# Kernel tuning notes

Hardware: AMD Instinct MI355X
Metric: run time of the kernel (lower is better)

The kernel has to match this reference:

```python
import jax, jax.numpy as jnp
import numpy as np

B, N, K = 4, 4096, 16
DP, DM = 64, 128
EPS = 1e-8


def setup_inputs() -> dict:
    key = jax.random.key(0)
    ks = jax.random.split(key, 32)
    g = lambda i, shape, fan: jax.random.normal(ks[i], shape, jnp.float32) / np.sqrt(fan)
    inp = {
        'xyz': jax.random.normal(ks[0], (B, N, 3), jnp.float32),
        'features': jax.random.normal(ks[1], (B, N, DP), jnp.float32),
        # fc1: d_points -> d_model
        'fc1_w': g(2, (DP, DM), DP), 'fc1_b': jnp.zeros((DM,), jnp.float32),
        # fc2: d_model -> d_points
        'fc2_w': g(3, (DM, DP), DM), 'fc2_b': jnp.zeros((DP,), jnp.float32),
        # fc_delta: Linear(3,DM) -> ReLU -> Linear(DM,DM)
        'd1_w': g(4, (3, DM), 3), 'd1_b': jnp.zeros((DM,), jnp.float32),
        'd2_w': g(5, (DM, DM), DM), 'd2_b': jnp.zeros((DM,), jnp.float32),
        # fc_gamma: Linear(DM,DM) -> ReLU -> Linear(DM,DM)
        'g1_w': g(6, (DM, DM), DM), 'g1_b': jnp.zeros((DM,), jnp.float32),
        'g2_w': g(7, (DM, DM), DM), 'g2_b': jnp.zeros((DM,), jnp.float32),
        # q/k/v projections, no bias
        'wq_w': g(8, (DM, DM), DM), 'wk_w': g(9, (DM, DM), DM), 'wv_w': g(10, (DM, DM), DM),
        # fc_sim: Linear(DM+1, DM)
        'sim_w': g(11, (DM + 1, DM), DM + 1), 'sim_b': jnp.zeros((DM,), jnp.float32),
    }
    return inp


def _gather(t, idx):
    # t: [B, N, C], idx: [B, N, K] -> [B, N, K, C]
    bidx = jnp.arange(t.shape[0])[:, None, None]
    return t[bidx, idx]


def reference(xyz, features, fc1_w, fc1_b, fc2_w, fc2_b, d1_w, d1_b, d2_w, d2_b,
              g1_w, g1_b, g2_w, g2_b, wq_w, wk_w, wv_w, sim_w, sim_b):
    # pairwise squared distances [B, N, N]
    sq = jnp.sum(xyz * xyz, axis=-1)
    dists = sq[:, :, None] + sq[:, None, :] - 2.0 * jnp.einsum('bnc,bmc->bnm', xyz, xyz)
    knn_idx = jnp.argsort(dists, axis=-1)[:, :, :K]            # [B, N, K]

    knn_xyz = _gather(xyz, knn_idx)                            # [B, N, K, 3]
    x = features @ fc1_w + fc1_b                               # [B, N, DM]
    q = x @ wq_w                                               # [B, N, DM]
    k = _gather(x @ wk_w, knn_idx)                             # [B, N, K, DM]
    v = _gather(x @ wv_w, knn_idx)                             # [B, N, K, DM]

    rel_pos = xyz[:, :, None, :] - knn_xyz                     # [B, N, K, 3]
    pos_enc = jax.nn.relu(rel_pos @ d1_w + d1_b) @ d2_w + d2_b # [B, N, K, DM]

    qe = q[:, :, None, :]                                      # [B, N, 1, DM]
    # torch cosine_similarity: dot / (max(||q||,eps) * max(||k||,eps))
    qn = jnp.maximum(jnp.linalg.norm(q, axis=-1), EPS)[:, :, None]
    kn = jnp.maximum(jnp.linalg.norm(k, axis=-1), EPS)
    sim = jnp.sum(qe * k, axis=-1) / (qn * kn)                 # [B, N, K]

    rel_qk = jnp.concatenate([sim[..., None], qe - k], axis=-1)  # [B, N, K, DM+1]
    rel_qk = rel_qk @ sim_w + sim_b                            # [B, N, K, DM]

    attn = jax.nn.relu((rel_qk + pos_enc) @ g1_w + g1_b) @ g2_w + g2_b
    attn = jax.nn.softmax(attn / np.sqrt(DM).astype(np.float32), axis=-2)  # over K

    res = jnp.einsum('bnkf,bnkf->bnf', attn, v + pos_enc)      # [B, N, DM]
    res = res @ fc2_w + fc2_b + features                       # [B, N, DP]
    return res, attn
```

## Files before the change

### kernel.cpp

```cpp
#include <hip/hip_runtime.h>
#include <hip/hip_bf16.h>

#define BB 4
#define NN 4096
#define KK 16
#define DP 64
#define DM 128
#define DMP 132
#define SPITCH 264
#define EPSF 1e-8f
#define OUT0N ((size_t)BB * NN * DP)

typedef unsigned short u16t;
typedef __attribute__((ext_vector_type(8))) short s8v;
typedef __attribute__((ext_vector_type(4))) float f4v;

__device__ int g_flag;

__device__ __forceinline__ float u2f(u16t u) {
    unsigned int x = ((unsigned int)u) << 16;
    return __uint_as_float(x);
}
__device__ __forceinline__ u16t f2u(float v) {
    __hip_bfloat16 h = __float2bfloat16(v);
    return *(u16t*)&h;
}
__device__ __forceinline__ void splitf(float x, u16t& h, u16t& l) {
    const unsigned xb = __float_as_uint(x);
    h = (u16t)(xb >> 16);
    const float hf = __uint_as_float(xb & 0xffff0000u);
    l = (u16t)(__float_as_uint(x - hf) >> 16);
}

template<int DT> struct IO;
template<> struct IO<0> {
    static __device__ __forceinline__ float ld(const void* p, size_t i) { return ((const float*)p)[i]; }
    static __device__ __forceinline__ void ld4(const void* p, size_t i, float o[4]) {
        float4 v = *(const float4*)((const float*)p + i);
        o[0] = v.x; o[1] = v.y; o[2] = v.z; o[3] = v.w;
    }
    static __device__ __forceinline__ void st(void* p, size_t i, float v) { ((float*)p)[i] = v; }
};
template<> struct IO<1> {
    static __device__ __forceinline__ float ld(const void* p, size_t i) { return u2f(((const u16t*)p)[i]); }
    static __device__ __forceinline__ void ld4(const void* p, size_t i, float o[4]) {
        ushort4 v = *(const ushort4*)((const u16t*)p + i);
        o[0] = u2f(v.x); o[1] = u2f(v.y); o[2] = u2f(v.z); o[3] = u2f(v.w);
    }
    static __device__ __forceinline__ void st(void* p, size_t i, float v) { ((u16t*)p)[i] = f2u(v); }
};

__global__ __launch_bounds__(64) void detect_kernel(const void* feat) {
    const int tid = threadIdx.x;
    float x = u2f(((const u16t*)feat)[2 * tid]);
    float a = fabsf(x);
    bool sane = (x == 0.0f) || (a > 1e-4f && a < 50.0f);
    unsigned long long m = __ballot(sane);
    if (tid == 0) g_flag = (__popcll(m) >= 32) ? 1 : 0;
}

struct QkvSmem { float sf[DP]; float sx[DM]; };

template<int DT>
__device__ __forceinline__ void qkv_body(QkvSmem& s,
    const void* feat, const void* fc1_w, const void* fc1_b,
    const void* wq, const void* wk, const void* wv,
    float* __restrict__ qbuf, float* __restrict__ kbuf, float* __restrict__ vbuf)
{
    const int bn = blockIdx.x;
    const int tid = threadIdx.x;
    if (tid < DP) s.sf[tid] = IO<DT>::ld(feat, (size_t)bn * DP + tid);
    __syncthreads();
    float x = IO<DT>::ld(fc1_b, tid);
#pragma unroll 4
    for (int i = 0; i < DP; i++) x = fmaf(s.sf[i], IO<DT>::ld(fc1_w, i * DM + tid), x);
    s.sx[tid] = x;
    __syncthreads();
    float q = 0.f, k = 0.f, v = 0.f;
    for (int i0 = 0; i0 < DM; i0 += 4) {
        float4 xv = *(const float4*)&s.sx[i0];
        const float xs[4] = { xv.x, xv.y, xv.z, xv.w };
#pragma unroll
        for (int j = 0; j < 4; j++) {
            q = fmaf(xs[j], IO<DT>::ld(wq, (i0 + j) * DM + tid), q);
            k = fmaf(xs[j], IO<DT>::ld(wk, (i0 + j) * DM + tid), k);
            v = fmaf(xs[j], IO<DT>::ld(wv, (i0 + j) * DM + tid), v);
        }
    }
    qbuf[(size_t)bn * DM + tid] = q;
    kbuf[(size_t)bn * DM + tid] = k;
    vbuf[(size_t)bn * DM + tid] = v;
}

__global__ __launch_bounds__(128) void qkv_kernel(
    const void* feat, const void* fc1_w, const void* fc1_b,
    const void* wq, const void* wk, const void* wv,
    float* qbuf, float* kbuf, float* vbuf)
{
    __shared__ __align__(16) QkvSmem s;
    if (g_flag) qkv_body<1>(s, feat, fc1_w, fc1_b, wq, wk, wv, qbuf, kbuf, vbuf);
    else        qkv_body<0>(s, feat, fc1_w, fc1_b, wq, wk, wv, qbuf, kbuf, vbuf);
}

struct Qkv16Smem { float sf[16][DP]; float sx[16][DMP]; };

template<int DT>
__device__ __forceinline__ void qkv16_body(Qkv16Smem& s,
    const void* feat, const void* fc1_w, const void* fc1_b,
    const void* wq, const void* wk, const void* wv,
    float* __restrict__ qbuf, float* __restrict__ kbuf, float* __restrict__ vbuf)
{
    const int pnt0 = blockIdx.x << 4;
    const int tid = threadIdx.x;
    {
        const int r = tid >> 4, c4 = (tid & 15) << 2;
        float o[4];
        IO<DT>::ld4(feat, (size_t)(pnt0 + r) * DP + c4, o);
        s.sf[r][c4 + 0] = o[0]; s.sf[r][c4 + 1] = o[1];
        s.sf[r][c4 + 2] = o[2]; s.sf[r][c4 + 3] = o[3];
    }
    __syncthreads();
    const int c = tid & 127, h = tid >> 7;
    {
        float acc[8];
        const float fb = IO<DT>::ld(fc1_b, c);
#pragma unroll
        for (int pp = 0; pp < 8; pp++) acc[pp] = fb;
        for (int i = 0; i < DP; i++) {
            const float w = IO<DT>::ld(fc1_w, (size_t)i * DM + c);
#pragma unroll
            for (int pp = 0; pp < 8; pp++) acc[pp] = fmaf(s.sf[h * 8 + pp][i], w, acc[pp]);
        }
#pragma unroll
        for (int pp = 0; pp < 8; pp++) s.sx[h * 8 + pp][c] = acc[pp];
    }
    __syncthreads();
    {
        float aq[8], ak[8], av[8];
#pragma unroll
        for (int pp = 0; pp < 8; pp++) { aq[pp] = 0.f; ak[pp] = 0.f; av[pp] = 0.f; }
        for (int i0 = 0; i0 < DM; i0 += 4) {
            float x4[8][4];
#pragma unroll
            for (int pp = 0; pp < 8; pp++) {
                const float4 xv = *(const float4*)&s.sx[h * 8 + pp][i0];
                x4[pp][0] = xv.x; x4[pp][1] = xv.y; x4[pp][2] = xv.z; x4[pp][3] = xv.w;
            }
#pragma unroll
            for (int j = 0; j < 4; j++) {
                const float wqv = IO<DT>::ld(wq, (size_t)(i0 + j) * DM + c);
                const float wkv = IO<DT>::ld(wk, (size_t)(i0 + j) * DM + c);
                const float wvv = IO<DT>::ld(wv, (size_t)(i0 + j) * DM + c);
#pragma unroll
                for (int pp = 0; pp < 8; pp++) {
                    aq[pp] = fmaf(x4[pp][j], wqv, aq[pp]);
                    ak[pp] = fmaf(x4[pp][j], wkv, ak[pp]);
                    av[pp] = fmaf(x4[pp][j], wvv, av[pp]);
                }
            }
        }
#pragma unroll
        for (int pp = 0; pp < 8; pp++) {
            const size_t row = (size_t)(pnt0 + h * 8 + pp) * DM + c;
            qbuf[row] = aq[pp]; kbuf[row] = ak[pp]; vbuf[row] = av[pp];
        }
    }
}

__global__ __launch_bounds__(256) void qkv16_kernel(
    const void* feat, const void* fc1_w, const void* fc1_b,
    const void* wq, const void* wk, const void* wv,
    float* qbuf, float* kbuf, float* vbuf)
{
    __shared__ __align__(16) Qkv16Smem s;
    if (g_flag) qkv16_body<1>(s, feat, fc1_w, fc1_b, wq, wk, wv, qbuf, kbuf, vbuf);
    else        qkv16_body<0>(s, feat, fc1_w, fc1_b, wq, wk, wv, qbuf, kbuf, vbuf);
}

template<int DT>
__device__ __forceinline__ void knn_body(float4* __restrict__ sc,
    const void* xyz, int* dst, int dstride, void* dout, int in_out)
{
    if (in_out) {
        if (DT) { dst = (int*)((u16t*)dout + OUT0N); dstride = (KK * DM) / 2; }
        else    { dst = (int*)((float*)dout + OUT0N); dstride = KK * DM; }
    }
    const int b = blockIdx.x >> 8;
    const int tid = threadIdx.x;
    for (int j = tid; j < NN; j += 512) {
        float x = IO<DT>::ld(xyz, ((size_t)b * NN + j) * 3 + 0);
        float y = IO<DT>::ld(xyz, ((size_t)b * NN + j) * 3 + 1);
        float z = IO<DT>::ld(xyz, ((size_t)b * NN + j) * 3 + 2);
        float sq = __fadd_rn(__fadd_rn(__fmul_rn(x, x), __fmul_rn(y, y)), __fmul_rn(z, z));
        sc[j] = make_float4(x, y, z, sq);
    }
    __syncthreads();
    const int lane = tid & 63;
    const int wave = tid >> 6;

    for (int qi = 0; qi < 2; qi++) {
        const int r = ((blockIdx.x & 255) << 4) + (wave << 1) + qi;
        const float4 qc = sc[r];

        float d[KK];
        int id[KK];
#pragma unroll
        for (int t = 0; t < KK; t++) { d[t] = 3.4e38f; id[t] = 0x7fffffff; }

        for (int j = lane; j < NN; j += 64) {
            const float4 c = sc[j];
            const float dot = __fadd_rn(__fadd_rn(__fmul_rn(qc.x, c.x), __fmul_rn(qc.y, c.y)),
                                        __fmul_rn(qc.z, c.z));
            const float dist = __fsub_rn(__fadd_rn(qc.w, c.w), __fmul_rn(2.0f, dot));
            if (dist < d[KK - 1]) {
                float cd = dist; int ci = j;
#pragma unroll
                for (int t = 0; t < KK; t++) {
                    const bool sw = (cd < d[t]);
                    const float od = d[t]; const int oi = id[t];
                    d[t]  = sw ? cd : d[t];
                    id[t] = sw ? ci : id[t];
                    cd = sw ? od : cd;
                    ci = sw ? oi : ci;
                }
            }
        }

        const size_t base = (size_t)(b * NN + r) * (size_t)dstride;
#pragma unroll
        for (int t = 0; t < KK; t++) {
            float bd = d[0]; int bi = id[0];
#pragma unroll
            for (int off = 32; off >= 1; off >>= 1) {
                const float od = __shfl_xor(bd, off, 64);
                const int   oi = __shfl_xor(bi, off, 64);
                if (od < bd || (od == bd && oi < bi)) { bd = od; bi = oi; }
            }
            const bool win = (d[0] == bd) && (id[0] == bi);
            if (win) {
#pragma unroll
                for (int u = 0; u < KK - 1; u++) { d[u] = d[u + 1]; id[u] = id[u + 1]; }
                d[KK - 1] = 3.4e38f; id[KK - 1] = 0x7fffffff;
            }
            if (lane == t) dst[base + t] = bi;
        }
    }
}

__global__ __launch_bounds__(512) void knn_kernel(
    const void* xyz, int* dst, int dstride, void* dout, int in_out)
{
    __shared__ __align__(16) float4 sc[NN];
    if (g_flag) knn_body<1>(sc, xyz, dst, dstride, dout, in_out);
    else        knn_body<0>(sc, xyz, dst, dstride, dout, in_out);
}

template<int DT>
__device__ __forceinline__ void gemm_tile(const float* __restrict__ IN,
                                          const void* __restrict__ W, int woff,
                                          int kg, int f0, float acc[4][4])
{
#pragma unroll
    for (int a = 0; a < 4; a++)
#pragma unroll
        for (int c = 0; c < 4; c++) acc[a][c] = 0.f;
    for (int i0 = 0; i0 < DM; i0 += 4) {
        float w[4][4];
#pragma unroll
        for (int j = 0; j < 4; j++) IO<DT>::ld4(W, (size_t)woff + (i0 + j) * DM + f0, w[j]);
#pragma unroll
        for (int kk = 0; kk < 4; kk++) {
            float4 x4 = *(const float4*)(IN + (kg * 4 + kk) * DMP + i0);
            const float xs[4] = { x4.x, x4.y, x4.z, x4.w };
#pragma unroll
            for (int ff = 0; ff < 4; ff++)
#pragma unroll
                for (int j = 0; j < 4; j++)
                    acc[kk][ff] = fmaf(xs[j], w[j][ff], acc[kk][ff]);
        }
    }
}

template<int DT>
__device__ __forceinline__ void wprep_body(const void* sim_w, const void* d2_w,
                                           const void* g1_w, const void* g2_w,
                                           u16t* __restrict__ wprep)
{
    const int m  = blockIdx.x >> 3;
    const int t  = blockIdx.x & 7;
    const int ks = threadIdx.x >> 6;
    const int lane = threadIdx.x & 63;
    const void* src = (m == 0) ? sim_w : (m == 1) ? d2_w : (m == 2) ? g1_w : g2_w;
    const int srcoff = (m == 0) ? DM : 0;
    u16t* hi = wprep + (size_t)m * 32768;
    u16t* lo = hi + 16384;
    const int c  = t * 16 + (lane & 15);
    const int k0 = ks * 32 + ((lane >> 4) << 3);
    s8v vh, vl;
#pragma unroll
    for (int j = 0; j < 8; j++) {
        const float x = IO<DT>::ld(src, (size_t)srcoff + (size_t)(k0 + j) * DM + c);
        const u16t h = f2u(x);
        vh[j] = (short)h;
        vl[j] = (short)f2u(x - u2f(h));
    }
    const size_t off = ((size_t)(t * 4 + ks) * 64 + lane) * 8;
    *(s8v*)(hi + off) = vh;
    *(s8v*)(lo + off) = vl;
}

__global__ __launch_bounds__(256) void wprep_kernel(
    const void* sim_w, const void* d2_w, const void* g1_w, const void* g2_w,
    u16t* wprep)
{
    if (g_flag) wprep_body<1>(sim_w, d2_w, g1_w, g2_w, wprep);
    else        wprep_body<0>(sim_w, d2_w, g1_w, g2_w, wprep);
}

__device__ __forceinline__ void mfma_g(const u16t* __restrict__ SP,
                                       const u16t* __restrict__ wmat,
                                       int lane, int w, f4v acc[4][2])
{
    const u16t* whi = wmat;
    const u16t* wlo = wmat + 16384;
    const int arow = lane & 15;
    const int ak   = (lane >> 4) << 3;
#pragma unroll
    for (int ks = 0; ks < 4; ks++) {
        const size_t o0 = ((size_t)(((2 * w + 0) * 4 + ks) * 64) + lane) * 8;
        const size_t o1 = ((size_t)(((2 * w + 1) * 4 + ks) * 64) + lane) * 8;
        const s8v b0h = *(const s8v*)(whi + o0);
        const s8v b0l = *(const s8v*)(wlo + o0);
        const s8v b1h = *(const s8v*)(whi + o1);
        const s8v b1l = *(const s8v*)(wlo + o1);
#pragma unroll
        for (int m = 0; m < 4; m++) {
            const u16t* ar = SP + (size_t)(m * 16 + arow) * SPITCH + ak + ks * 32;
            const s8v ah = *(const s8v*)ar;
            const s8v al = *(const s8v*)(ar + 128);
            acc[m][0] = __builtin_amdgcn_mfma_f32_16x16x32_bf16(ah, b0h, acc[m][0], 0, 0, 0);
            acc[m][0] = __builtin_amdgcn_mfma_f32_16x16x32_bf16(ah, b0l, acc[m][0], 0, 0, 0);
            acc[m][0] = __builtin_amdgcn_mfma_f32_16x16x32_bf16(al, b0h, acc[m][0], 0, 0, 0);
            acc[m][1] = __builtin_amdgcn_mfma_f32_16x16x32_bf16(ah, b1h, acc[m][1], 0, 0, 0);
            acc[m][1] = __builtin_amdgcn_mfma_f32_16x16x32_bf16(ah, b1l, acc[m][1], 0, 0, 0);
            acc[m][1] = __builtin_amdgcn_mfma_f32_16x16x32_bf16(al, b1h, acc[m][1], 0, 0, 0);
        }
    }
}

struct Attn5Smem {
    u16t  SP[64 * SPITCH];
    float sq[4][DM];
    float sres[4][DM];
    float ssim[64];
};

template<int DT>
__device__ __forceinline__ void attn5_body(Attn5Smem& s,
    const void* xyz, const void* feat,
    const void* fc2_w, const void* fc2_b,
    const void* d1_w, const void* d1_b, const void* d2_b,
    const void* g1_b, const void* g2_b,
    const void* sim_w, const void* sim_b,
    const float* __restrict__ qbuf, const float* __restrict__ kbuf,
    const float* __restrict__ vbuf,
    const int* __restrict__ knn, const u16t* __restrict__ wprep, void* dout)
{
    void* out0 = dout;
    void* out1 = DT ? (void*)((u16t*)dout + OUT0N) : (void*)((float*)dout + OUT0N);
    const int pnt0 = blockIdx.x << 2;
    const int b = pnt0 >> 12;
    const int tid = threadIdx.x;
    const int lane = tid & 63;
    const int w = tid >> 6;
    const int h = lane >> 4;
    const int c = lane & 15;
    const int row = tid >> 2;
    const int cb  = (tid & 3) << 5;

    int sv = knn[(size_t)(pnt0 + w) * KK + (row & 15)];
    sv = (sv < 0) ? 0 : (sv > NN - 1 ? NN - 1 : sv);
    const int grow = (b << 12) + sv;
    const float rx = IO<DT>::ld(xyz, (size_t)(pnt0 + w) * 3 + 0) - IO<DT>::ld(xyz, (size_t)grow * 3 + 0);
    const float ry = IO<DT>::ld(xyz, (size_t)(pnt0 + w) * 3 + 1) - IO<DT>::ld(xyz, (size_t)grow * 3 + 1);
    const float rz = IO<DT>::ld(xyz, (size_t)(pnt0 + w) * 3 + 2) - IO<DT>::ld(xyz, (size_t)grow * 3 + 2);
    float4 kreg[8];
#pragma unroll
    for (int j4 = 0; j4 < 8; j4++)
        kreg[j4] = *(const float4*)&kbuf[(size_t)grow * DM + cb + 4 * j4];
    const float2 q2 = *(const float2*)&qbuf[(size_t)(pnt0 + w) * DM + lane * 2];
    *(float2*)&s.sq[w][lane * 2] = q2;
    float qq = fmaf(q2.x, q2.x, q2.y * q2.y);
#pragma unroll
    for (int off = 1; off <= 32; off <<= 1) qq += __shfl_xor(qq, off, 64);
    const float qn = fmaxf(sqrtf(qq), EPSF);

    {
        u16t* hp = &s.SP[row * SPITCH];
#pragma unroll
        for (int j4 = 0; j4 < 32; j4 += 4) {
            float w0[4], w1[4], w2[4], bb[4];
            IO<DT>::ld4(d1_w, (size_t)0 * DM + cb + j4, w0);
            IO<DT>::ld4(d1_w, (size_t)1 * DM + cb + j4, w1);
            IO<DT>::ld4(d1_w, (size_t)2 * DM + cb + j4, w2);
            IO<DT>::ld4(d1_b, cb + j4, bb);
            ushort4 hv, lv;
#pragma unroll
            for (int jj = 0; jj < 4; jj++) {
                const float hx = fmaxf(fmaf(rz, w2[jj], fmaf(ry, w1[jj], fmaf(rx, w0[jj], bb[jj]))), 0.f);
                u16t hs, ls; splitf(hx, hs, ls);
                ((u16t*)&hv)[jj] = hs; ((u16t*)&lv)[jj] = ls;
            }
            *(ushort4*)(hp + cb + j4) = hv;
            *(ushort4*)(hp + 128 + cb + j4) = lv;
        }
    }
    __syncthreads();

    f4v pe[4][2] = { { {0,0,0,0},{0,0,0,0} }, { {0,0,0,0},{0,0,0,0} },
                     { {0,0,0,0},{0,0,0,0} }, { {0,0,0,0},{0,0,0,0} } };
    mfma_g(s.SP, wprep + 1 * 32768, lane, w, pe);
#pragma unroll
    for (int nt = 0; nt < 2; nt++) {
        const float bv = IO<DT>::ld(d2_b, (2 * w + nt) * 16 + c);
#pragma unroll
        for (int m = 0; m < 4; m++)
#pragma unroll
            for (int r = 0; r < 4; r++) pe[m][nt][r] += bv;
    }
    {
        float sk = 0.f, sd = 0.f;
#pragma unroll
        for (int j4 = 0; j4 < 8; j4++) {
            const float4 kv = kreg[j4];
            const float4 qv = *(const float4*)&s.sq[w][cb + 4 * j4];
            sk = fmaf(kv.x, kv.x, fmaf(kv.y, kv.y, fmaf(kv.z, kv.z, fmaf(kv.w, kv.w, sk))));
            sd = fmaf(qv.x, kv.x, fmaf(qv.y, kv.y, fmaf(qv.z, kv.z, fmaf(qv.w, kv.w, sd))));
        }
        sk += __shfl_xor(sk, 1, 64); sk += __shfl_xor(sk, 2, 64);
        sd += __shfl_xor(sd, 1, 64); sd += __shfl_xor(sd, 2, 64);
        if ((tid & 3) == 0) {
            const float kn = fmaxf(sqrtf(sk), EPSF);
            s.ssim[row] = sd / (qn * kn);
        }
    }
    __syncthreads();

    {
        u16t* hp = &s.SP[row * SPITCH];
#pragma unroll
        for (int j4 = 0; j4 < 8; j4++) {
            const float4 kv = kreg[j4];
            const float4 qv = *(const float4*)&s.sq[w][cb + 4 * j4];
            ushort4 hv, lv;
            splitf(qv.x - kv.x, hv.x, lv.x);
            splitf(qv.y - kv.y, hv.y, lv.y);
            splitf(qv.z - kv.z, hv.z, lv.z);
            splitf(qv.w - kv.w, hv.w, lv.w);
            *(ushort4*)(hp + cb + 4 * j4) = hv;
            *(ushort4*)(hp + 128 + cb + 4 * j4) = lv;
        }
    }
    __syncthreads();

    {
        f4v a1[4][2] = { { {0,0,0,0},{0,0,0,0} }, { {0,0,0,0},{0,0,0,0} },
                         { {0,0,0,0},{0,0,0,0} }, { {0,0,0,0},{0,0,0,0} } };
        mfma_g(s.SP, wprep + 0 * 32768, lane, w, a1);
        __syncthreads();
#pragma unroll
        for (int nt = 0; nt < 2; nt++) {
            const int col = (2 * w + nt) * 16 + c;
            const float bv  = IO<DT>::ld(sim_b, col);
            const float w0v = IO<DT>::ld(sim_w, col);
#pragma unroll
            for (int m = 0; m < 4; m++)
#pragma unroll
                for (int r = 0; r < 4; r++) {
                    const int rr = m * 16 + 4 * h + r;
                    const float val = a1[m][nt][r] + bv + s.ssim[rr] * w0v + pe[m][nt][r];
                    u16t hs, ls; splitf(val, hs, ls);
                    s.SP[(size_t)rr * SPITCH + col] = hs;
                    s.SP[(size_t)rr * SPITCH + 128 + col] = ls;
                }
        }
    }
    __syncthreads();

    {
        f4v a3[4][2] = { { {0,0,0,0},{0,0,0,0} }, { {0,0,0,0},{0,0,0,0} },
                         { {0,0,0,0},{0,0,0,0} }, { {0,0,0,0},{0,0,0,0} } };
        mfma_g(s.SP, wprep + 2 * 32768, lane, w, a3);
        __syncthreads();
#pragma unroll
        for (int nt = 0; nt < 2; nt++) {
            const int col = (2 * w + nt) * 16 + c;
            const float bv = IO<DT>::ld(g1_b, col);
#pragma unroll
            for (int m = 0; m < 4; m++)
#pragma unroll
                for (int r = 0; r < 4; r++) {
                    const int rr = m * 16 + 4 * h + r;
                    const float val = fmaxf(a3[m][nt][r] + bv, 0.f);
                    u16t hs, ls; splitf(val, hs, ls);
                    s.SP[(size_t)rr * SPITCH + col] = hs;
                    s.SP[(size_t)rr * SPITCH + 128 + col] = ls;
                }
        }
    }
    __syncthreads();

    f4v av[4][2];
    float4 vreg[8];
    {
        f4v a4[4][2] = { { {0,0,0,0},{0,0,0,0} }, { {0,0,0,0},{0,0,0,0} },
                         { {0,0,0,0},{0,0,0,0} }, { {0,0,0,0},{0,0,0,0} } };
        mfma_g(s.SP, wprep + 3 * 32768, lane, w, a4);
        const float inv = 0.08838834764831843f;
#pragma unroll
        for (int nt = 0; nt < 2; nt++) {
            const int col = (2 * w + nt) * 16 + c;
            const float bv = IO<DT>::ld(g2_b, col);
#pragma unroll
            for (int m = 0; m < 4; m++) {
                float tv[4];
#pragma unroll
                for (int r = 0; r < 4; r++) tv[r] = (a4[m][nt][r] + bv) * inv;
                float mx = fmaxf(fmaxf(tv[0], tv[1]), fmaxf(tv[2], tv[3]));
                mx = fmaxf(mx, __shfl_xor(mx, 16, 64));
                mx = fmaxf(mx, __shfl_xor(mx, 32, 64));
                float ssum = 0.f;
#pragma unroll
                for (int r = 0; r < 4; r++) { tv[r] = __expf(tv[r] - mx); ssum += tv[r]; }
                ssum += __shfl_xor(ssum, 16, 64);
                ssum += __shfl_xor(ssum, 32, 64);
                const float rs = 1.0f / ssum;
#pragma unroll
                for (int r = 0; r < 4; r++) {
                    const float a = tv[r] * rs;
                    av[m][nt][r] = a;
                    IO<DT>::st(out1, ((size_t)(pnt0 + m) * KK + (4 * h + r)) * DM + col, a);
                }
            }
        }
#pragma unroll
        for (int nt = 0; nt < 2; nt++) {
            const int col = (2 * w + nt) * 16 + c;
#pragma unroll
            for (int m = 0; m < 4; m++) {
                float pd = 0.f;
#pragma unroll
                for (int r = 0; r < 4; r++) pd = fmaf(av[m][nt][r], pe[m][nt][r], pd);
                pd += __shfl_xor(pd, 16, 64);
                pd += __shfl_xor(pd, 32, 64);
                if (h == 0) s.sres[m][col] = pd;
            }
        }
#pragma unroll
        for (int j4 = 0; j4 < 8; j4++)
            vreg[j4] = *(const float4*)&vbuf[(size_t)grow * DM + cb + 4 * j4];
    }
    __syncthreads();

    float* vst = (float*)s.SP;
#pragma unroll
    for (int j4 = 0; j4 < 8; j4++)
        *(float4*)&vst[row * 132 + cb + 4 * j4] = vreg[j4];
    __syncthreads();
    {
#pragma unroll
        for (int nt = 0; nt < 2; nt++) {
            const int col = (2 * w + nt) * 16 + c;
#pragma unroll
            for (int m = 0; m < 4; m++) {
                float part = 0.f;
#pragma unroll
                for (int r = 0; r < 4; r++)
                    part = fmaf(av[m][nt][r], vst[(m * 16 + 4 * h + r) * 132 + col], part);
                part += __shfl_xor(part, 16, 64);
                part += __shfl_xor(part, 32, 64);
                if (h == 0) s.sres[m][col] += part;
            }
        }
    }
    __syncthreads();

    {
        const int pt = tid >> 6, cc = tid & 63;
        float o = 0.f;
        for (int i = 0; i < DM; i++)
            o = fmaf(s.sres[pt][i], IO<DT>::ld(fc2_w, (size_t)i * DP + cc), o);
        o = o + IO<DT>::ld(fc2_b, cc) + IO<DT>::ld(feat, (size_t)(pnt0 + pt) * DP + cc);
        IO<DT>::st(out0, (size_t)(pnt0 + pt) * DP + cc, o);
    }
}

__global__ __launch_bounds__(256, 4) void attn5_kernel(
    const void* xyz, const void* feat,
    const void* fc2_w, const void* fc2_b,
    const void* d1_w, const void* d1_b, const void* d2_b,
    const void* g1_b, const void* g2_b,
    const void* sim_w, const void* sim_b,
    const float* qbuf, const float* kbuf, const float* vbuf,
    const int* knn, const u16t* wprep, void* dout)
{
    __shared__ __align__(16) Attn5Smem s;
    if (g_flag)
        attn5_body<1>(s, xyz, feat, fc2_w, fc2_b, d1_w, d1_b, d2_b, g1_b, g2_b,
                      sim_w, sim_b, qbuf, kbuf, vbuf, knn, wprep, dout);
    else
        attn5_body<0>(s, xyz, feat, fc2_w, fc2_b, d1_w, d1_b, d2_b, g1_b, g2_b,
                      sim_w, sim_b, qbuf, kbuf, vbuf, knn, wprep, dout);
}

template<bool FUSED> struct AttnSmem {
    float Kb[KK * DMP], Vb[KK * DMP], PE[KK * DMP], T0[KK * DMP], T1[KK * DMP];
    float s_q[DM], sres[DM];
    float SF[FUSED ? 17 * DP : 1];
    float X[FUSED ? 17 * DMP : 1];
    float srp[KK][3];
    float ssim[KK], skn[KK], sdot[KK];
    float sqn;
    int sidx[KK];
};

template<int DT, bool FUSED>
__device__ __forceinline__ void attn_body(AttnSmem<FUSED>& s,
    const void* xyz, const void* feat,
    const void* fc1_w, const void* fc1_b, const void* fc2_w, const void* fc2_b,
    const void* d1_w, const void* d1_b, const void* d2_w, const void* d2_b,
    const void* g1_w, const void* g1_b, const void* g2_w, const void* g2_b,
    const void* sim_w, const void* sim_b,
    const void* wq, const void* wk, const void* wv,
    const float* __restrict__ qbuf, const float* __restrict__ kbuf, const float* __restrict__ vbuf,
    const int* knn, int knn_stride, int knn_in_out, void* dout)
{
    void* out0 = dout;
    void* out1 = DT ? (void*)((u16t*)dout + OUT0N) : (void*)((float*)dout + OUT0N);
    if (knn_in_out) {
        if (DT) { knn = (const int*)((const u16t*)dout + OUT0N); knn_stride = (KK * DM) / 2; }
        else    { knn = (const int*)((const float*)dout + OUT0N); knn_stride = KK * DM; }
    }

    const int bn = blockIdx.x;
    const int b = bn >> 12;
    const int tid = threadIdx.x;
    const int f = tid;
    const int f0 = (tid & 31) * 4;
    const int kg = tid >> 5;

    if (tid < KK) {
        int sv = knn[(size_t)bn * knn_stride + tid];
        sv = (sv < 0) ? 0 : (sv > NN - 1 ? NN - 1 : sv);
        s.sidx[tid] = sv;
    }
    __syncthreads();

    if constexpr (FUSED) {
        for (int idx = tid; idx < 17 * DP; idx += 128) {
            const int r = idx >> 6, c = idx & 63;
            const int row = (r < KK) ? ((b << 12) + s.sidx[r]) : bn;
            s.SF[idx] = IO<DT>::ld(feat, (size_t)row * DP + c);
        }
        __syncthreads();
        float xacc[17];
        const float fb = IO<DT>::ld(fc1_b, tid);
#pragma unroll
        for (int r = 0; r < 17; r++) xacc[r] = fb;
        for (int i = 0; i < DP; i++) {
            const float w = IO<DT>::ld(fc1_w, i * DM + tid);
#pragma unroll
            for (int r = 0; r < 17; r++) xacc[r] = fmaf(s.SF[r * DP + i], w, xacc[r]);
        }
#pragma unroll
        for (int r = 0; r < 17; r++) s.X[r * DMP + tid] = xacc[r];
        __syncthreads();
        {
            float a2[4][4];
            gemm_tile<DT>(s.X, wk, 0, kg, f0, a2);
#pragma unroll
            for (int kk = 0; kk < 4; kk++)
                *(float4*)&s.Kb[(kg * 4 + kk) * DMP + f0] =
                    make_float4(a2[kk][0], a2[kk][1], a2[kk][2], a2[kk][3]);
            gemm_tile<DT>(s.X, wv, 0, kg, f0, a2);
#pragma unroll
            for (int kk = 0; kk < 4; kk++)
                *(float4*)&s.Vb[(kg * 4 + kk) * DMP + f0] =
                    make_float4(a2[kk][0], a2[kk][1], a2[kk][2], a2[kk][3]);
        }
        {
            float qv = 0.f;
            for (int i0 = 0; i0 < DM; i0 += 4) {
                float4 x4 = *(const float4*)&s.X[16 * DMP + i0];
                const float xs[4] = { x4.x, x4.y, x4.z, x4.w };
#pragma unroll
                for (int j = 0; j < 4; j++)
                    qv = fmaf(xs[j], IO<DT>::ld(wq, (i0 + j) * DM + tid), qv);
            }
            s.s_q[tid] = qv;
        }
    } else {
        s.s_q[f] = qbuf[(size_t)bn * DM + f];
#pragma unroll
        for (int k = 0; k < KK; k++) {
            const int row = (b << 12) + s.sidx[k];
            s.Kb[k * DMP + f] = kbuf[(size_t)row * DM + f];
            s.Vb[k * DMP + f] = vbuf[(size_t)row * DM + f];
        }
    }
    if (tid < KK) {
        const int row = (b << 12) + s.sidx[tid];
#pragma unroll
        for (int c = 0; c < 3; c++)
            s.srp[tid][c] = IO<DT>::ld(xyz, (size_t)bn * 3 + c) - IO<DT>::ld(xyz, (size_t)row * 3 + c);
    }
    __syncthreads();

    if (tid < KK) {
        float sk = 0.f, sd = 0.f;
        for (int i = 0; i < DM; i++) {
            float v2 = s.Kb[tid * DMP + i];
            sk = fmaf(v2, v2, sk);
            sd = fmaf(s.s_q[i], v2, sd);
        }
        s.skn[tid] = fmaxf(sqrtf(sk), EPSF);
        s.sdot[tid] = sd;
    } else if (tid == KK) {
        float sqq = 0.f;
        for (int i = 0; i < DM; i++) { float v2 = s.s_q[i]; sqq = fmaf(v2, v2, sqq); }
        s.sqn = fmaxf(sqrtf(sqq), EPSF);
    }
    __syncthreads();
    if (tid < KK) s.ssim[tid] = s.sdot[tid] / (s.sqn * s.skn[tid]);
#pragma unroll
    for (int k = 0; k < KK; k++) s.T0[k * DMP + f] = s.s_q[f] - s.Kb[k * DMP + f];
    __syncthreads();

    float acc[4][4];

    gemm_tile<DT>(s.T0, sim_w, DM, kg, f0, acc);
    {
        float w0f[4], sbf[4];
        IO<DT>::ld4(sim_w, f0, w0f);
        IO<DT>::ld4(sim_b, f0, sbf);
#pragma unroll
        for (int kk = 0; kk < 4; kk++) {
            float sm = s.ssim[kg * 4 + kk];
            float4 o;
            o.x = fmaf(sm, w0f[0], acc[kk][0]) + sbf[0];
            o.y = fmaf(sm, w0f[1], acc[kk][1]) + sbf[1];
            o.z = fmaf(sm, w0f[2], acc[kk][2]) + sbf[2];
            o.w = fmaf(sm, w0f[3], acc[kk][3]) + sbf[3];
            *(float4*)&s.T1[(kg * 4 + kk) * DMP + f0] = o;
        }
    }
    __syncthreads();

    {
        float w0 = IO<DT>::ld(d1_w, 0 * DM + f), w1 = IO<DT>::ld(d1_w, 1 * DM + f),
              w2 = IO<DT>::ld(d1_w, 2 * DM + f);
        float hb = IO<DT>::ld(d1_b, f);
#pragma unroll
        for (int k = 0; k < KK; k++) {
            float h = fmaf(s.srp[k][2], w2, fmaf(s.srp[k][1], w1, fmaf(s.srp[k][0], w0, hb)));
            s.T0[k * DMP + f] = fmaxf(h, 0.f);
        }
    }
    __syncthreads();

    gemm_tile<DT>(s.T0, d2_w, 0, kg, f0, acc);
    {
        float bf[4];
        IO<DT>::ld4(d2_b, f0, bf);
#pragma unroll
        for (int kk = 0; kk < 4; kk++)
            *(float4*)&s.PE[(kg * 4 + kk) * DMP + f0] =
                make_float4(acc[kk][0] + bf[0], acc[kk][1] + bf[1],
                            acc[kk][2] + bf[2], acc[kk][3] + bf[3]);
    }
    __syncthreads();

#pragma unroll
    for (int kk = 0; kk < 4; kk++) {
        const int row = (kg * 4 + kk) * DMP + f0;
        float4 a4 = *(const float4*)&s.T1[row];
        float4 p4 = *(const float4*)&s.PE[row];
        *(float4*)&s.T0[row] = make_float4(a4.x + p4.x, a4.y + p4.y, a4.z + p4.z, a4.w + p4.w);
    }
    __syncthreads();

    gemm_tile<DT>(s.T0, g1_w, 0, kg, f0, acc);
    {
        float bf[4];
        IO<DT>::ld4(g1_b, f0, bf);
#pragma unroll
        for (int kk = 0; kk < 4; kk++)
            *(float4*)&s.T1[(kg * 4 + kk) * DMP + f0] =
                make_float4(fmaxf(acc[kk][0] + bf[0], 0.f), fmaxf(acc[kk][1] + bf[1], 0.f),
                            fmaxf(acc[kk][2] + bf[2], 0.f), fmaxf(acc[kk][3] + bf[3], 0.f));
    }
    __syncthreads();

    gemm_tile<DT>(s.T1, g2_w, 0, kg, f0, acc);
    {
        float bf[4];
        IO<DT>::ld4(g2_b, f0, bf);
#pragma unroll
        for (int kk = 0; kk < 4; kk++)
            *(float4*)&s.T0[(kg * 4 + kk) * DMP + f0] =
                make_float4(acc[kk][0] + bf[0], acc[kk][1] + bf[1],
                            acc[kk][2] + bf[2], acc[kk][3] + bf[3]);
    }
    __syncthreads();

    {
        const float sq128 = 11.31370849898476f;
        float tv[KK];
        float m = -3.4e38f;
#pragma unroll
        for (int k = 0; k < KK; k++) { tv[k] = s.T0[k * DMP + f] / sq128; m = fmaxf(m, tv[k]); }
        float ssum = 0.f;
#pragma unroll
        for (int k = 0; k < KK; k++) { tv[k] = expf(tv[k] - m); ssum += tv[k]; }
        float rf = 0.f;
#pragma unroll
        for (int k = 0; k < KK; k++) {
            float a = tv[k] / ssum;
            IO<DT>::st(out1, ((size_t)bn * KK + k) * DM + f, a);
            rf = fmaf(a, s.Vb[k * DMP + f] + s.PE[k * DMP + f], rf);
        }
        s.sres[f] = rf;
    }
    __syncthreads();

    if (tid < DP) {
        float o = 0.f;
        for (int i = 0; i < DM; i++) o = fmaf(s.sres[i], IO<DT>::ld(fc2_w, i * DP + tid), o);
        o = o + IO<DT>::ld(fc2_b, tid) + IO<DT>::ld(feat, (size_t)bn * DP + tid);
        IO<DT>::st(out0, (size_t)bn * DP + tid, o);
    }
}

template<bool FUSED>
__global__ __launch_bounds__(128) void attn_kernel(
    const void* xyz, const void* feat,
    const void* fc1_w, const void* fc1_b, const void* fc2_w, const void* fc2_b,
    const void* d1_w, const void* d1_b, const void* d2_w, const void* d2_b,
    const void* g1_w, const void* g1_b, const void* g2_w, const void* g2_b,
    const void* sim_w, const void* sim_b,
    const void* wq, const void* wk, const void* wv,
    const float* qbuf, const float* kbuf, const float* vbuf,
    const int* knn, int knn_stride, int knn_in_out, void* dout)
{
    __shared__ __align__(16) AttnSmem<FUSED> s;
    if (g_flag)
        attn_body<1, FUSED>(s, xyz, feat, fc1_w, fc1_b, fc2_w, fc2_b, d1_w, d1_b, d2_w, d2_b,
                            g1_w, g1_b, g2_w, g2_b, sim_w, sim_b, wq, wk, wv,
                            qbuf, kbuf, vbuf, knn, knn_stride, knn_in_out, dout);
    else
        attn_body<0, FUSED>(s, xyz, feat, fc1_w, fc1_b, fc2_w, fc2_b, d1_w, d1_b, d2_w, d2_b,
                            g1_w, g1_b, g2_w, g2_b, sim_w, sim_b, wq, wk, wv,
                            qbuf, kbuf, vbuf, knn, knn_stride, knn_in_out, dout);
}

extern "C" void kernel_launch(void* const* d_in, const int* in_sizes, int n_in,
                              void* d_out, int out_size, void* d_ws, size_t ws_size,
                              hipStream_t stream)
{
    const void* xyz   = d_in[0];
    const void* feat  = d_in[1];
    const void* fc1_w = d_in[2];
    const void* fc1_b = d_in[3];
    const void* fc2_w = d_in[4];
    const void* fc2_b = d_in[5];
    const void* d1_w  = d_in[6];
    const void* d1_b  = d_in[7];
    const void* d2_w  = d_in[8];
    const void* d2_b  = d_in[9];
    const void* g1_w  = d_in[10];
    const void* g1_b  = d_in[11];
    const void* g2_w  = d_in[12];
    const void* g2_b  = d_in[13];
    const void* wq_w  = d_in[14];
    const void* wk_w  = d_in[15];
    const void* wv_w  = d_in[16];
    const void* sim_w = d_in[17];
    const void* sim_b = d_in[18];

    detect_kernel<<<1, 64, 0, stream>>>(feat);

    const size_t need_qkv = (size_t)3 * BB * NN * DM * sizeof(float);
    const size_t need_knn = (size_t)BB * NN * KK * sizeof(int);
    const size_t need_wp  = (size_t)4 * 2 * 16384 * sizeof(u16t);

    if (ws_size >= need_qkv + need_knn + need_wp && d_ws != nullptr) {
        float* qbuf  = (float*)d_ws;
        float* kbuf  = qbuf + (size_t)BB * NN * DM;
        float* vbuf  = kbuf + (size_t)BB * NN * DM;
        int*   knn   = (int*)(vbuf + (size_t)BB * NN * DM);
        u16t*  wprep = (u16t*)(knn + (size_t)BB * NN * KK);
        qkv16_kernel<<<(BB * NN) / 16, 256, 0, stream>>>(feat, fc1_w, fc1_b, wq_w, wk_w, wv_w,
                                                         qbuf, kbuf, vbuf);
        knn_kernel<<<BB * 256, 512, 0, stream>>>(xyz, knn, KK, d_out, 0);
        wprep_kernel<<<32, 256, 0, stream>>>(sim_w, d2_w, g1_w, g2_w, wprep);
        attn5_kernel<<<(BB * NN) / 4, 256, 0, stream>>>(
            xyz, feat, fc2_w, fc2_b, d1_w, d1_b, d2_b, g1_b, g2_b, sim_w, sim_b,
            qbuf, kbuf, vbuf, knn, wprep, d_out);
    } else if (ws_size >= need_qkv + need_knn && d_ws != nullptr) {
        float* qbuf = (float*)d_ws;
        float* kbuf = qbuf + (size_t)BB * NN * DM;
        float* vbuf = kbuf + (size_t)BB * NN * DM;
        int*   knn  = (int*)(vbuf + (size_t)BB * NN * DM);
        qkv_kernel<<<BB * NN, DM, 0, stream>>>(feat, fc1_w, fc1_b, wq_w, wk_w, wv_w, qbuf, kbuf, vbuf);
        knn_kernel<<<BB * 256, 512, 0, stream>>>(xyz, knn, KK, d_out, 0);
        attn_kernel<false><<<BB * NN, DM, 0, stream>>>(
            xyz, feat, fc1_w, fc1_b, fc2_w, fc2_b, d1_w, d1_b, d2_w, d2_b,
            g1_w, g1_b, g2_w, g2_b, sim_w, sim_b, wq_w, wk_w, wv_w,
            qbuf, kbuf, vbuf, knn, KK, 0, d_out);
    } else if (ws_size >= need_knn && d_ws != nullptr) {
        int* knn = (int*)d_ws;
        knn_kernel<<<BB * 256, 512, 0, stream>>>(xyz, knn, KK, d_out, 0);
        attn_kernel<true><<<BB * NN, DM, 0, stream>>>(
            xyz, feat, fc1_w, fc1_b, fc2_w, fc2_b, d1_w, d1_b, d2_w, d2_b,
            g1_w, g1_b, g2_w, g2_b, sim_w, sim_b, wq_w, wk_w, wv_w,
            nullptr, nullptr, nullptr, knn, KK, 0, d_out);
    } else {
        knn_kernel<<<BB * 256, 512, 0, stream>>>(xyz, nullptr, 0, d_out, 1);
        attn_kernel<true><<<BB * NN, DM, 0, stream>>>(
            xyz, feat, fc1_w, fc1_b, fc2_w, fc2_b, d1_w, d1_b, d2_w, d2_b,
            g1_w, g1_b, g2_w, g2_b, sim_w, sim_b, wq_w, wk_w, wv_w,
            nullptr, nullptr, nullptr, nullptr, 0, 1, d_out);
    }
}
```

Baseline: 648.5 us.

## Merge qkv, knn and weight-prep into one launch and halve knn work per block

Replaces the three separate preparation kernels (qkv projection, kNN search, MFMA weight repacking) with a single prep_kernel that dispatches on block index, so independent work runs concurrently instead of back to back. The kNN part now has each wave handle one query point instead of two, doubling the block count to spread the serial search across more CUs. The qkv part uses 512-thread blocks with 4 points per thread half instead of 8. The cost is that each kNN block reloads all point coordinates into LDS for only 8 queries, and the merged kernel's LDS union (64KB) limits occupancy for the qkv blocks.

```diff
diff --git a/kernel.cpp b/kernel.cpp
--- a/kernel.cpp
+++ b/kernel.cpp
@@ -102,81 +102,6 @@
     else        qkv_body<0>(s, feat, fc1_w, fc1_b, wq, wk, wv, qbuf, kbuf, vbuf);
 }
 
-struct Qkv16Smem { float sf[16][DP]; float sx[16][DMP]; };
-
-template<int DT>
-__device__ __forceinline__ void qkv16_body(Qkv16Smem& s,
-    const void* feat, const void* fc1_w, const void* fc1_b,
-    const void* wq, const void* wk, const void* wv,
-    float* __restrict__ qbuf, float* __restrict__ kbuf, float* __restrict__ vbuf)
-{
-    const int pnt0 = blockIdx.x << 4;
-    const int tid = threadIdx.x;
-    {
-        const int r = tid >> 4, c4 = (tid & 15) << 2;
-        float o[4];
-        IO<DT>::ld4(feat, (size_t)(pnt0 + r) * DP + c4, o);
-        s.sf[r][c4 + 0] = o[0]; s.sf[r][c4 + 1] = o[1];
-        s.sf[r][c4 + 2] = o[2]; s.sf[r][c4 + 3] = o[3];
-    }
-    __syncthreads();
-    const int c = tid & 127, h = tid >> 7;
-    {
-        float acc[8];
-        const float fb = IO<DT>::ld(fc1_b, c);
-#pragma unroll
-        for (int pp = 0; pp < 8; pp++) acc[pp] = fb;
-        for (int i = 0; i < DP; i++) {
-            const float w = IO<DT>::ld(fc1_w, (size_t)i * DM + c);
-#pragma unroll
-            for (int pp = 0; pp < 8; pp++) acc[pp] = fmaf(s.sf[h * 8 + pp][i], w, acc[pp]);
-        }
-#pragma unroll
-        for (int pp = 0; pp < 8; pp++) s.sx[h * 8 + pp][c] = acc[pp];
-    }
-    __syncthreads();
-    {
-        float aq[8], ak[8], av[8];
-#pragma unroll
-        for (int pp = 0; pp < 8; pp++) { aq[pp] = 0.f; ak[pp] = 0.f; av[pp] = 0.f; }
-        for (int i0 = 0; i0 < DM; i0 += 4) {
-            float x4[8][4];
-#pragma unroll
-            for (int pp = 0; pp < 8; pp++) {
-                const float4 xv = *(const float4*)&s.sx[h * 8 + pp][i0];
-                x4[pp][0] = xv.x; x4[pp][1] = xv.y; x4[pp][2] = xv.z; x4[pp][3] = xv.w;
-            }
-#pragma unroll
-            for (int j = 0; j < 4; j++) {
-                const float wqv = IO<DT>::ld(wq, (size_t)(i0 + j) * DM + c);
-                const float wkv = IO<DT>::ld(wk, (size_t)(i0 + j) * DM + c);
-                const float wvv = IO<DT>::ld(wv, (size_t)(i0 + j) * DM + c);
-#pragma unroll
-                for (int pp = 0; pp < 8; pp++) {
-                    aq[pp] = fmaf(x4[pp][j], wqv, aq[pp]);
-                    ak[pp] = fmaf(x4[pp][j], wkv, ak[pp]);
-                    av[pp] = fmaf(x4[pp][j], wvv, av[pp]);
-                }
-            }
-        }
-#pragma unroll
-        for (int pp = 0; pp < 8; pp++) {
-            const size_t row = (size_t)(pnt0 + h * 8 + pp) * DM + c;
-            qbuf[row] = aq[pp]; kbuf[row] = ak[pp]; vbuf[row] = av[pp];
-        }
-    }
-}
-
-__global__ __launch_bounds__(256) void qkv16_kernel(
-    const void* feat, const void* fc1_w, const void* fc1_b,
-    const void* wq, const void* wk, const void* wv,
-    float* qbuf, float* kbuf, float* vbuf)
-{
-    __shared__ __align__(16) Qkv16Smem s;
-    if (g_flag) qkv16_body<1>(s, feat, fc1_w, fc1_b, wq, wk, wv, qbuf, kbuf, vbuf);
-    else        qkv16_body<0>(s, feat, fc1_w, fc1_b, wq, wk, wv, qbuf, kbuf, vbuf);
-}
-
 template<int DT>
 __device__ __forceinline__ void knn_body(float4* __restrict__ sc,
     const void* xyz, int* dst, int dstride, void* dout, int in_out)
@@ -185,7 +110,7 @@
         if (DT) { dst = (int*)((u16t*)dout + OUT0N); dstride = (KK * DM) / 2; }
         else    { dst = (int*)((float*)dout + OUT0N); dstride = KK * DM; }
     }
-    const int b = blockIdx.x >> 8;
+    const int b = blockIdx.x >> 9;
     const int tid = threadIdx.x;
     for (int j = tid; j < NN; j += 512) {
         float x = IO<DT>::ld(xyz, ((size_t)b * NN + j) * 3 + 0);
@@ -197,53 +122,50 @@
     __syncthreads();
     const int lane = tid & 63;
     const int wave = tid >> 6;
-
-    for (int qi = 0; qi < 2; qi++) {
-        const int r = ((blockIdx.x & 255) << 4) + (wave << 1) + qi;
-        const float4 qc = sc[r];
-
-        float d[KK];
-        int id[KK];
-#pragma unroll
-        for (int t = 0; t < KK; t++) { d[t] = 3.4e38f; id[t] = 0x7fffffff; }
-
-        for (int j = lane; j < NN; j += 64) {
-            const float4 c = sc[j];
-            const float dot = __fadd_rn(__fadd_rn(__fmul_rn(qc.x, c.x), __fmul_rn(qc.y, c.y)),
-                                        __fmul_rn(qc.z, c.z));
-            const float dist = __fsub_rn(__fadd_rn(qc.w, c.w), __fmul_rn(2.0f, dot));
-            if (dist < d[KK - 1]) {
-                float cd = dist; int ci = j;
-#pragma unroll
-                for (int t = 0; t < KK; t++) {
-                    const bool sw = (cd < d[t]);
-                    const float od = d[t]; const int oi = id[t];
-                    d[t]  = sw ? cd : d[t];
-                    id[t] = sw ? ci : id[t];
-                    cd = sw ? od : cd;
-                    ci = sw ? oi : ci;
-                }
+    const int r = ((blockIdx.x & 511) << 3) + wave;
+    const float4 qc = sc[r];
+
+    float d[KK];
+    int id[KK];
+#pragma unroll
+    for (int t = 0; t < KK; t++) { d[t] = 3.4e38f; id[t] = 0x7fffffff; }
+
+    for (int j = lane; j < NN; j += 64) {
+        const float4 c = sc[j];
+        const float dot = __fadd_rn(__fadd_rn(__fmul_rn(qc.x, c.x), __fmul_rn(qc.y, c.y)),
+                                    __fmul_rn(qc.z, c.z));
+        const float dist = __fsub_rn(__fadd_rn(qc.w, c.w), __fmul_rn(2.0f, dot));
+        if (dist < d[KK - 1]) {
+            float cd = dist; int ci = j;
+#pragma unroll
+            for (int t = 0; t < KK; t++) {
+                const bool sw = (cd < d[t]);
+                const float od = d[t]; const int oi = id[t];
+                d[t]  = sw ? cd : d[t];
+                id[t] = sw ? ci : id[t];
+                cd = sw ? od : cd;
+                ci = sw ? oi : ci;
             }
         }
-
-        const size_t base = (size_t)(b * NN + r) * (size_t)dstride;
-#pragma unroll
-        for (int t = 0; t < KK; t++) {
-            float bd = d[0]; int bi = id[0];
-#pragma unroll
-            for (int off = 32; off >= 1; off >>= 1) {
-                const float od = __shfl_xor(bd, off, 64);
-                const int   oi = __shfl_xor(bi, off, 64);
-                if (od < bd || (od == bd && oi < bi)) { bd = od; bi = oi; }
-            }
-            const bool win = (d[0] == bd) && (id[0] == bi);
-            if (win) {
-#pragma unroll
-                for (int u = 0; u < KK - 1; u++) { d[u] = d[u + 1]; id[u] = id[u + 1]; }
-                d[KK - 1] = 3.4e38f; id[KK - 1] = 0x7fffffff;
-            }
-            if (lane == t) dst[base + t] = bi;
-        }
+    }
+
+    const size_t base = (size_t)(b * NN + r) * (size_t)dstride;
+#pragma unroll
+    for (int t = 0; t < KK; t++) {
+        float bd = d[0]; int bi = id[0];
+#pragma unroll
+        for (int off = 32; off >= 1; off >>= 1) {
+            const float od = __shfl_xor(bd, off, 64);
+            const int   oi = __shfl_xor(bi, off, 64);
+            if (od < bd || (od == bd && oi < bi)) { bd = od; bi = oi; }
+        }
+        const bool win = (d[0] == bd) && (id[0] == bi);
+        if (win) {
+#pragma unroll
+            for (int u = 0; u < KK - 1; u++) { d[u] = d[u + 1]; id[u] = id[u + 1]; }
+            d[KK - 1] = 3.4e38f; id[KK - 1] = 0x7fffffff;
+        }
+        if (lane == t) dst[base + t] = bi;
     }
 }
 
@@ -255,40 +177,150 @@
     else        knn_body<0>(sc, xyz, dst, dstride, dout, in_out);
 }
 
+#define PREP_QKV_BLKS ((BB * NN) / 16)
+#define PREP_KNN_BLKS (BB * 512)
+#define PREP_WP_BLKS  16
+#define PREP_BLKS (PREP_QKV_BLKS + PREP_KNN_BLKS + PREP_WP_BLKS)
+
+struct PrepSmem {
+    union {
+        float4 sc[NN];
+        struct { float sf[16][DP]; float sx[16][DMP]; } q;
+    };
+};
+
 template<int DT>
-__device__ __forceinline__ void gemm_tile(const float* __restrict__ IN,
-                                          const void* __restrict__ W, int woff,
-                                          int kg, int f0, float acc[4][4])
-{
-#pragma unroll
-    for (int a = 0; a < 4; a++)
-#pragma unroll
-        for (int c = 0; c < 4; c++) acc[a][c] = 0.f;
-    for (int i0 = 0; i0 < DM; i0 += 4) {
-        float w[4][4];
-#pragma unroll
-        for (int j = 0; j < 4; j++) IO<DT>::ld4(W, (size_t)woff + (i0 + j) * DM + f0, w[j]);
-#pragma unroll
-        for (int kk = 0; kk < 4; kk++) {
-            float4 x4 = *(const float4*)(IN + (kg * 4 + kk) * DMP + i0);
-            const float xs[4] = { x4.x, x4.y, x4.z, x4.w };
-#pragma unroll
-            for (int ff = 0; ff < 4; ff++)
-#pragma unroll
-                for (int j = 0; j < 4; j++)
-                    acc[kk][ff] = fmaf(xs[j], w[j][ff], acc[kk][ff]);
+__device__ __forceinline__ void qkv512_body(PrepSmem& s, int qblk,
+    const void* feat, const void* fc1_w, const void* fc1_b,
+    const void* wq, const void* wk, const void* wv,
+    float* __restrict__ qbuf, float* __restrict__ kbuf, float* __restrict__ vbuf)
+{
+    const int pnt0 = qblk << 4;
+    const int tid = threadIdx.x;
+    {
+        const int r = tid >> 5, c2 = (tid & 31) << 1;
+        s.q.sf[r][c2]     = IO<DT>::ld(feat, (size_t)(pnt0 + r) * DP + c2);
+        s.q.sf[r][c2 + 1] = IO<DT>::ld(feat, (size_t)(pnt0 + r) * DP + c2 + 1);
+    }
+    __syncthreads();
+    const int c = tid & 127, h = tid >> 7;
+    {
+        float acc[4];
+        const float fb = IO<DT>::ld(fc1_b, c);
+#pragma unroll
+        for (int pp = 0; pp < 4; pp++) acc[pp] = fb;
+        for (int i = 0; i < DP; i++) {
+            const float w = IO<DT>::ld(fc1_w, (size_t)i * DM + c);
+#pragma unroll
+            for (int pp = 0; pp < 4; pp++) acc[pp] = fmaf(s.q.sf[h * 4 + pp][i], w, acc[pp]);
+        }
+#pragma unroll
+        for (int pp = 0; pp < 4; pp++) s.q.sx[h * 4 + pp][c] = acc[pp];
+    }
+    __syncthreads();
+    {
+        float aq[4], ak[4], av[4];
+#pragma unroll
+        for (int pp = 0; pp < 4; pp++) { aq[pp] = 0.f; ak[pp] = 0.f; av[pp] = 0.f; }
+        for (int i0 = 0; i0 < DM; i0 += 4) {
+            float x4[4][4];
+#pragma unroll
+            for (int pp = 0; pp < 4; pp++) {
+                const float4 xv = *(const float4*)&s.q.sx[h * 4 + pp][i0];
+                x4[pp][0] = xv.x; x4[pp][1] = xv.y; x4[pp][2] = xv.z; x4[pp][3] = xv.w;
+            }
+#pragma unroll
+            for (int j = 0; j < 4; j++) {
+                const float wqv = IO<DT>::ld(wq, (size_t)(i0 + j) * DM + c);
+                const float wkv = IO<DT>::ld(wk, (size_t)(i0 + j) * DM + c);
+                const float wvv = IO<DT>::ld(wv, (size_t)(i0 + j) * DM + c);
+#pragma unroll
+                for (int pp = 0; pp < 4; pp++) {
+                    aq[pp] = fmaf(x4[pp][j], wqv, aq[pp]);
+                    ak[pp] = fmaf(x4[pp][j], wkv, ak[pp]);
+                    av[pp] = fmaf(x4[pp][j], wvv, av[pp]);
+                }
+            }
+        }
+#pragma unroll
+        for (int pp = 0; pp < 4; pp++) {
+            const size_t row = (size_t)(pnt0 + h * 4 + pp) * DM + c;
+            qbuf[row] = aq[pp]; kbuf[row] = ak[pp]; vbuf[row] = av[pp];
         }
     }
 }
 
 template<int DT>
-__device__ __forceinline__ void wprep_body(const void* sim_w, const void* d2_w,
-                                           const void* g1_w, const void* g2_w,
-                                           u16t* __restrict__ wprep)
-{
-    const int m  = blockIdx.x >> 3;
-    const int t  = blockIdx.x & 7;
-    const int ks = threadIdx.x >> 6;
+__device__ __forceinline__ void knn512_body(float4* __restrict__ sc, int kblk,
+    const void* xyz, int* __restrict__ dst)
+{
+    const int b = kblk >> 9;
+    const int tid = threadIdx.x;
+    for (int j = tid; j < NN; j += 512) {
+        float x = IO<DT>::ld(xyz, ((size_t)b * NN + j) * 3 + 0);
+        float y = IO<DT>::ld(xyz, ((size_t)b * NN + j) * 3 + 1);
+        float z = IO<DT>::ld(xyz, ((size_t)b * NN + j) * 3 + 2);
+        float sq = __fadd_rn(__fadd_rn(__fmul_rn(x, x), __fmul_rn(y, y)), __fmul_rn(z, z));
+        sc[j] = make_float4(x, y, z, sq);
+    }
+    __syncthreads();
+    const int lane = tid & 63;
+    const int wave = tid >> 6;
+    const int r = ((kblk & 511) << 3) + wave;
+    const float4 qc = sc[r];
+
+    float d[KK];
+    int id[KK];
+#pragma unroll
+    for (int t = 0; t < KK; t++) { d[t] = 3.4e38f; id[t] = 0x7fffffff; }
+
+    for (int j = lane; j < NN; j += 64) {
+        const float4 c = sc[j];
+        const float dot = __fadd_rn(__fadd_rn(__fmul_rn(qc.x, c.x), __fmul_rn(qc.y, c.y)),
+                                    __fmul_rn(qc.z, c.z));
+        const float dist = __fsub_rn(__fadd_rn(qc.w, c.w), __fmul_rn(2.0f, dot));
+        if (dist < d[KK - 1]) {
+            float cd = dist; int ci = j;
+#pragma unroll
+            for (int t = 0; t < KK; t++) {
+                const bool sw = (cd < d[t]);
+                const float od = d[t]; const int oi = id[t];
+                d[t]  = sw ? cd : d[t];
+                id[t] = sw ? ci : id[t];
+                cd = sw ? od : cd;
+                ci = sw ? oi : ci;
+            }
+        }
+    }
+
+    const size_t base = (size_t)(b * NN + r) * (size_t)KK;
+#pragma unroll
+    for (int t = 0; t < KK; t++) {
+        float bd = d[0]; int bi = id[0];
+#pragma unroll
+        for (int off = 32; off >= 1; off >>= 1) {
+            const float od = __shfl_xor(bd, off, 64);
+            const int   oi = __shfl_xor(bi, off, 64);
+            if (od < bd || (od == bd && oi < bi)) { bd = od; bi = oi; }
+        }
+        const bool win = (d[0] == bd) && (id[0] == bi);
+        if (win) {
+#pragma unroll
+            for (int u = 0; u < KK - 1; u++) { d[u] = d[u + 1]; id[u] = id[u + 1]; }
+            d[KK - 1] = 3.4e38f; id[KK - 1] = 0x7fffffff;
+        }
+        if (lane == t) dst[base + t] = bi;
+    }
+}
+
+template<int DT>
+__device__ __forceinline__ void wprep512_body(int wblk,
+    const void* sim_w, const void* d2_w, const void* g1_w, const void* g2_w,
+    u16t* __restrict__ wprep)
+{
+    const int m  = wblk >> 2;
+    const int t  = ((wblk & 3) << 1) + (threadIdx.x >> 8);
+    const int ks = (threadIdx.x >> 6) & 3;
     const int lane = threadIdx.x & 63;
     const void* src = (m == 0) ? sim_w : (m == 1) ? d2_w : (m == 2) ? g1_w : g2_w;
     const int srcoff = (m == 0) ? DM : 0;
@@ -309,12 +341,64 @@
     *(s8v*)(lo + off) = vl;
 }
 
-__global__ __launch_bounds__(256) void wprep_kernel(
+template<int DT>
+__device__ __forceinline__ void prep_body(PrepSmem& s,
+    const void* xyz, const void* feat,
+    const void* fc1_w, const void* fc1_b,
+    const void* wq, const void* wk, const void* wv,
     const void* sim_w, const void* d2_w, const void* g1_w, const void* g2_w,
-    u16t* wprep)
-{
-    if (g_flag) wprep_body<1>(sim_w, d2_w, g1_w, g2_w, wprep);
-    else        wprep_body<0>(sim_w, d2_w, g1_w, g2_w, wprep);
+    float* qbuf, float* kbuf, float* vbuf, int* knnbuf, u16t* wprep)
+{
+    const int blk = blockIdx.x;
+    if (blk < PREP_QKV_BLKS) {
+        qkv512_body<DT>(s, blk, feat, fc1_w, fc1_b, wq, wk, wv, qbuf, kbuf, vbuf);
+    } else if (blk < PREP_QKV_BLKS + PREP_KNN_BLKS) {
+        knn512_body<DT>(s.sc, blk - PREP_QKV_BLKS, xyz, knnbuf);
+    } else {
+        wprep512_body<DT>(blk - PREP_QKV_BLKS - PREP_KNN_BLKS, sim_w, d2_w, g1_w, g2_w, wprep);
+    }
+}
+
+__global__ __launch_bounds__(512) void prep_kernel(
+    const void* xyz, const void* feat,
+    const void* fc1_w, const void* fc1_b,
+    const void* wq, const void* wk, const void* wv,
+    const void* sim_w, const void* d2_w, const void* g1_w, const void* g2_w,
+    float* qbuf, float* kbuf, float* vbuf, int* knnbuf, u16t* wprep)
+{
+    __shared__ __align__(16) PrepSmem s;
+    if (g_flag)
+        prep_body<1>(s, xyz, feat, fc1_w, fc1_b, wq, wk, wv,
+                     sim_w, d2_w, g1_w, g2_w, qbuf, kbuf, vbuf, knnbuf, wprep);
+    else
+        prep_body<0>(s, xyz, feat, fc1_w, fc1_b, wq, wk, wv,
+                     sim_w, d2_w, g1_w, g2_w, qbuf, kbuf, vbuf, knnbuf, wprep);
+}
+
+template<int DT>
+__device__ __forceinline__ void gemm_tile(const float* __restrict__ IN,
+                                          const void* __restrict__ W, int woff,
+                                          int kg, int f0, float acc[4][4])
+{
+#pragma unroll
+    for (int a = 0; a < 4; a++)
+#pragma unroll
+        for (int c = 0; c < 4; c++) acc[a][c] = 0.f;
+    for (int i0 = 0; i0 < DM; i0 += 4) {
+        float w[4][4];
+#pragma unroll
+        for (int j = 0; j < 4; j++) IO<DT>::ld4(W, (size_t)woff + (i0 + j) * DM + f0, w[j]);
+#pragma unroll
+        for (int kk = 0; kk < 4; kk++) {
+            float4 x4 = *(const float4*)(IN + (kg * 4 + kk) * DMP + i0);
+            const float xs[4] = { x4.x, x4.y, x4.z, x4.w };
+#pragma unroll
+            for (int ff = 0; ff < 4; ff++)
+#pragma unroll
+                for (int j = 0; j < 4; j++)
+                    acc[kk][ff] = fmaf(xs[j], w[j][ff], acc[kk][ff]);
+        }
+    }
 }
 
 __device__ __forceinline__ void mfma_g(const u16t* __restrict__ SP,
@@ -899,10 +983,9 @@
         float* vbuf  = kbuf + (size_t)BB * NN * DM;
         int*   knn   = (int*)(vbuf + (size_t)BB * NN * DM);
         u16t*  wprep = (u16t*)(knn + (size_t)BB * NN * KK);
-        qkv16_kernel<<<(BB * NN) / 16, 256, 0, stream>>>(feat, fc1_w, fc1_b, wq_w, wk_w, wv_w,
-                                                         qbuf, kbuf, vbuf);
-        knn_kernel<<<BB * 256, 512, 0, stream>>>(xyz, knn, KK, d_out, 0);
-        wprep_kernel<<<32, 256, 0, stream>>>(sim_w, d2_w, g1_w, g2_w, wprep);
+        prep_kernel<<<PREP_BLKS, 512, 0, stream>>>(
+            xyz, feat, fc1_w, fc1_b, wq_w, wk_w, wv_w,
+            sim_w, d2_w, g1_w, g2_w, qbuf, kbuf, vbuf, knn, wprep);
         attn5_kernel<<<(BB * NN) / 4, 256, 0, stream>>>(
             xyz, feat, fc2_w, fc2_b, d1_w, d1_b, d2_b, g1_b, g2_b, sim_w, sim_b,
             qbuf, kbuf, vbuf, knn, wprep, d_out);
@@ -912,20 +995,20 @@
         float* vbuf = kbuf + (size_t)BB * NN * DM;
         int*   knn  = (int*)(vbuf + (size_t)BB * NN * DM);
         qkv_kernel<<<BB * NN, DM, 0, stream>>>(feat, fc1_w, fc1_b, wq_w, wk_w, wv_w, qbuf, kbuf, vbuf);
-        knn_kernel<<<BB * 256, 512, 0, stream>>>(xyz, knn, KK, d_out, 0);
+        knn_kernel<<<BB * 512, 512, 0, stream>>>(xyz, knn, KK, d_out, 0);
         attn_kernel<false><<<BB * NN, DM, 0, stream>>>(
             xyz, feat, fc1_w, fc1_b, fc2_w, fc2_b, d1_w, d1_b, d2_w, d2_b,
             g1_w, g1_b, g2_w, g2_b, sim_w, sim_b, wq_w, wk_w, wv_w,
             qbuf, kbuf, vbuf, knn, KK, 0, d_out);
     } else if (ws_size >= need_knn && d_ws != nullptr) {
         int* knn = (int*)d_ws;
-        knn_kernel<<<BB * 256, 512, 0, stream>>>(xyz, knn, KK, d_out, 0);
+        knn_kernel<<<BB * 512, 512, 0, stream>>>(xyz, knn, KK, d_out, 0);
         attn_kernel<true><<<BB * NN, DM, 0, stream>>>(
             xyz, feat, fc1_w, fc1_b, fc2_w, fc2_b, d1_w, d1_b, d2_w, d2_b,
             g1_w, g1_b, g2_w, g2_b, sim_w, sim_b, wq_w, wk_w, wv_w,
             nullptr, nullptr, nullptr, knn, KK, 0, d_out);
     } else {
-        knn_kernel<<<BB * 256, 512, 0, stream>>>(xyz, nullptr, 0, d_out, 1);
+        knn_kernel<<<BB * 512, 512, 0, stream>>>(xyz, nullptr, 0, d_out, 1);
         attn_kernel<true><<<BB * NN, DM, 0, stream>>>(
             xyz, feat, fc1_w, fc1_b, fc2_w, fc2_b, d1_w, d1_b, d2_w, d2_b,
             g1_w, g1_b, g2_w, g2_b, sim_w, sim_b, wq_w, wk_w, wv_w,
```

New measurement: 590.1 us. -9.0%, faster.
